# Kernel optimization log

Measured on AMD Instinct MI355X. Metric: run time of the kernel, lower is better.

The kernel has to match this reference:

```python
import jax, jax.numpy as jnp
import numpy as np
import math

B, S, HID, L, NH, V, M = 8, 512, 768, 12, 12, 30522, 512
FF = 4 * HID
D = HID // NH


def sinusoidal_pe(seq_len, dim):
    pos = np.arange(seq_len, dtype=np.float32)[:, None]
    i = np.arange(dim // 2, dtype=np.float32)[None, :]
    ang = pos / np.power(10000.0, 2.0 * i / dim)
    pe = np.zeros((seq_len, dim), np.float32)
    pe[:, 0::2] = np.sin(ang)
    pe[:, 1::2] = np.cos(ang)
    return jnp.asarray(pe)


def setup_inputs() -> dict:
    key = jax.random.key(0)
    ks = iter(jax.random.split(key, 32))
    g = lambda sh: jax.random.normal(next(ks), sh, jnp.float32) * 0.02
    return {
        "token_ids": jax.random.randint(next(ks), (B, S), 0, V),
        "segment_info": jax.random.randint(next(ks), (B, S), 0, 2),
        "tok_emb": g((V, HID)),
        "seg_emb": g((3, HID)),
        "Wq": g((L, HID, HID)), "bq": jnp.zeros((L, HID)),
        "Wk": g((L, HID, HID)), "bk": jnp.zeros((L, HID)),
        "Wv": g((L, HID, HID)), "bv": jnp.zeros((L, HID)),
        "Wo": g((L, HID, HID)), "bo": jnp.zeros((L, HID)),
        "Wpk": g((L, HID, HID)),
        "Wpq": g((L, HID, HID)),
        "rel_emb": g((L, 2 * M, HID)),
        "ln1_g": jnp.ones((L, HID)), "ln1_b": jnp.zeros((L, HID)),
        "ln2_g": jnp.ones((L, HID)), "ln2_b": jnp.zeros((L, HID)),
        "W1": g((L, HID, FF)), "b1": jnp.zeros((L, FF)),
        "W2": g((L, FF, HID)), "b2": jnp.zeros((L, HID)),
        "lnf_g": jnp.ones((HID,)), "lnf_b": jnp.zeros((HID,)),
    }


def _ln(x, g, b):
    mu = x.mean(-1, keepdims=True)
    var = ((x - mu) ** 2).mean(-1, keepdims=True)
    return (x - mu) * jax.lax.rsqrt(var + 1e-5) * g + b


def _forward(token_ids, segment_info, tok_emb, seg_emb, layer_params, lnf_g, lnf_b):
    mask = token_ids != 0  # [B,S] valid-key mask
    x = tok_emb[token_ids] + sinusoidal_pe(S, HID)[None] + seg_emb[segment_info]
    qidx = jnp.arange(S)[:, None]
    # relative position bucket: clamp(q-k, -M, M-1) + M  -> [0, 2M)
    rel = jnp.clip(qidx - jnp.arange(S)[None, :], -M, M - 1) + M  # [S,S]
    scale = 1.0 / math.sqrt(3.0 * D)  # DeBERTa scales by sqrt(3d) for 3 score terms

    def body(x, p):
        (Wq, bq, Wk, bk, Wv, bv, Wo, bo, Wpk, Wpq, rel_e,
         l1g, l1b, l2g, l2b, W1, b1, W2, b2) = p
        # pre-norm attention sublayer
        h = _ln(x, l1g, l1b)
        q = (h @ Wq + bq).reshape(B, S, NH, D)
        k = (h @ Wk + bk).reshape(B, S, NH, D)
        v = (h @ Wv + bv).reshape(B, S, NH, D)
        c2c = jnp.einsum('bqhd,bkhd->bhqk', q, k)
        pk = (rel_e @ Wpk).reshape(2 * M, NH, D)
        pq = (rel_e @ Wpq).reshape(2 * M, NH, D)
        # content-to-position: Q_q . posK[rel(q,k)]
        c2p = jnp.einsum('bqhd,rhd->bhqr', q, pk)[:, :, qidx, rel]  # [B,NH,S,S]
        # position-to-content: K_k . posQ[rel(k,q)] -> gather over k rows then transpose
        p2c = jnp.einsum('bkhd,rhd->bhkr', k, pq)[:, :, qidx, rel]  # [B,NH,k,q]
        scores = (c2c + c2p + jnp.swapaxes(p2c, -1, -2)) * scale
        scores = jnp.where(mask[:, None, None, :], scores, -1e9)
        attn = jax.nn.softmax(scores, axis=-1)
        ctx = jnp.einsum('bhqk,bkhd->bqhd', attn, v).reshape(B, S, HID)
        x = x + ctx @ Wo + bo
        # pre-norm feedforward sublayer
        h2 = _ln(x, l2g, l2b)
        x = x + jax.nn.gelu(h2 @ W1 + b1, approximate=False) @ W2 + b2
        return x, None

    x, _ = jax.lax.scan(body, x, layer_params)
    return _ln(x, lnf_g, lnf_b)


def reference(token_ids, segment_info, tok_emb, seg_emb, Wq, bq, Wk, bk, Wv, bv,
              Wo, bo, Wpk, Wpq, rel_emb, ln1_g, ln1_b, ln2_g, ln2_b,
              W1, b1, W2, b2, lnf_g, lnf_b):
    lp = (Wq, bq, Wk, bk, Wv, bv, Wo, bo, Wpk, Wpq, rel_emb,
          ln1_g, ln1_b, ln2_g, ln2_b, W1, b1, W2, b2)
    return _forward(token_ids, segment_info, tok_emb, seg_emb, lp, lnf_g, lnf_b)
```

## Files before the change

kernel.cpp:

```cpp
#include <hip/hip_runtime.h>
#include <hip/hip_bf16.h>
#include <cstddef>
#include <cstdint>


constexpr int B   = 8;
constexpr int S   = 512;
constexpr int HID = 768;
constexpr int L   = 12;
constexpr int NH  = 12;
constexpr int D   = 64;
constexpr int FF  = 3072;
constexpr int M2  = 1024;
constexpr int NTOK = B * S;

using f32x4 = __attribute__((ext_vector_type(4))) float;
using s16x8 = __attribute__((ext_vector_type(8))) short;
typedef unsigned short us;

__device__ inline float wave_sum(float v) {
#pragma unroll
  for (int o = 32; o > 0; o >>= 1) v += __shfl_xor(v, o, 64);
  return v;
}
__device__ inline us f2bf(float f) {
  __hip_bfloat16 h = __float2bfloat16(f);
  return *reinterpret_cast<us*>(&h);
}
__device__ inline float bf2f(us u) {
  union { unsigned int i; float f; } x;
  x.i = ((unsigned int)u) << 16;
  return x.f;
}
__device__ inline int swz8(int row, int g) {
  return row * 64 + ((g ^ (row & 7)) << 3);
}
#define GLOAD16(gp, lp)                                                  \
  __builtin_amdgcn_global_load_lds(                                     \
      (const __attribute__((address_space(1))) void*)(gp),              \
      (__attribute__((address_space(3))) void*)(lp), 16, 0, 0)

__global__ void embed_kernel(const int* __restrict__ tok,
                             const int* __restrict__ seg,
                             const float* __restrict__ tok_emb,
                             const float* __restrict__ seg_emb,
                             float* __restrict__ x) {
  int row = blockIdx.x;
  int s = row & (S - 1);
  int t = tok[row];
  int sg = seg[row];
  for (int c = threadIdx.x; c < HID; c += blockDim.x) {
    int i = c >> 1;
    float ang = (float)s * powf(10000.0f, -2.0f * (float)i / (float)HID);
    float pe = (c & 1) ? cosf(ang) : sinf(ang);
    x[(size_t)row * HID + c] = tok_emb[(size_t)t * HID + c] + pe
                             + seg_emb[(size_t)sg * HID + c];
  }
}

template <int BF16OUT>
__global__ __launch_bounds__(256)
void ln_kernel(const float* __restrict__ in, void* __restrict__ outp,
               const float* __restrict__ g, const float* __restrict__ b,
               int nrows) {
  int wave = threadIdx.x >> 6, lane = threadIdx.x & 63;
  int row = blockIdx.x * 4 + wave;
  if (row >= nrows) return;
  const float* xr = in + (size_t)row * HID;
  float v[12];
  float s = 0.f;
#pragma unroll
  for (int i = 0; i < 12; i++) { v[i] = xr[lane + i * 64]; s += v[i]; }
  s = wave_sum(s);
  float mu = s * (1.0f / HID);
  float ss = 0.f;
#pragma unroll
  for (int i = 0; i < 12; i++) { float d = v[i] - mu; ss += d * d; }
  ss = wave_sum(ss);
  float inv = rsqrtf(ss * (1.0f / HID) + 1e-5f);
#pragma unroll
  for (int i = 0; i < 12; i++) {
    int c = lane + i * 64;
    float o = (v[i] - mu) * inv * g[c] + b[c];
    if (BF16OUT)
      ((us*)outp)[(size_t)row * HID + c] = f2bf(o);
    else
      ((float*)outp)[(size_t)row * HID + c] = o;
  }
}

__global__ __launch_bounds__(256)
void weight_prep(const float* Wq, const float* Wk, const float* Wv,
                 const float* Wo, const float* Wpk, const float* Wpq,
                 const float* W1s, const float* W2s, const float* rel,
                 us* __restrict__ wt6, us* __restrict__ wt1,
                 us* __restrict__ wt2, us* __restrict__ rel16) {
  int bz = blockIdx.x;
  if (bz >= 8064) {
    int i = (bz - 8064) * 1024 + threadIdx.x * 4;
    f32x4 v = *(const f32x4*)&rel[i];
#pragma unroll
    for (int j = 0; j < 4; j++) rel16[i + j] = f2bf(v[j]);
    return;
  }
  __shared__ float tile[32][33];
  int tx = threadIdx.x & 31, ty = threadIdx.x >> 5;
  const float* src;
  us* dst;
  int N, K, nt, kt;
  if (bz < 3456) {
    int z = bz / 576, r = bz % 576;
    const float* srcs[6] = {Wq, Wk, Wv, Wo, Wpk, Wpq};
    src = srcs[z];
    dst = wt6 + (size_t)z * HID * HID;
    N = HID; K = HID;
    nt = (r % 24) * 32; kt = (r / 24) * 32;
  } else if (bz < 5760) {
    int r = bz - 3456;
    src = W1s; dst = wt1; N = FF; K = HID;
    nt = (r % 96) * 32; kt = (r / 96) * 32;
  } else {
    int r = bz - 5760;
    src = W2s; dst = wt2; N = HID; K = FF;
    nt = (r % 24) * 32; kt = (r / 24) * 32;
  }
#pragma unroll
  for (int i = 0; i < 4; i++)
    tile[ty + i * 8][tx] = src[(size_t)(kt + ty + i * 8) * N + nt + tx];
  __syncthreads();
#pragma unroll
  for (int i = 0; i < 4; i++)
    dst[(size_t)(nt + ty + i * 8) * K + kt + tx] = f2bf(tile[tx][ty + i * 8]);
}

__global__ void concat_bias(const float* __restrict__ bq,
                            const float* __restrict__ bk,
                            const float* __restrict__ bv,
                            float* __restrict__ bqkv) {
  int i = blockIdx.x * 256 + threadIdx.x;
  if (i >= L * 2304) return;
  int l = i / 2304, c = i % 2304;
  float v = (c < 768) ? bq[l * 768 + c]
          : (c < 1536) ? bk[l * 768 + c - 768] : bv[l * 768 + c - 1536];
  bqkv[i] = v;
}

template <int TN, int OUT_BF16, int GELU, int PARTIAL>
__global__ __launch_bounds__(256)
void mfma_gemm(const us* __restrict__ A, const us* __restrict__ Bt,
               const float* __restrict__ bias, const float* __restrict__ res,
               void* __restrict__ C, int Mr, int K, int N, int Kc) {
  constexpr int NW = TN / 32;
  __shared__ us As[128 * 32];
  __shared__ us Bs[TN * 32];
  int t = threadIdx.x, wave = t >> 6, lane = t & 63;
  int r0 = blockIdx.y * 128, n0 = blockIdx.x * TN;
  int kb = blockIdx.z * Kc;
  int wr = (wave >> 1) * 64;
  int wc = (wave & 1) * (TN / 2);

  f32x4 acc[4][NW] = {};
  int srow = lane >> 2, selem = (lane & 3) * 8;

  for (int k0 = kb; k0 < kb + Kc; k0 += 32) {
    __syncthreads();
    {
      const us* gA = A + (size_t)(r0 + wave * 32 + srow) * K + k0 + selem;
      us* lA = &As[(wave * 32) * 32];
      GLOAD16(gA, lA);
      GLOAD16(gA + (size_t)16 * K, lA + 16 * 32);
      if (TN == 128) {
        const us* gB = Bt + (size_t)(n0 + wave * 32 + srow) * K + k0 + selem;
        us* lB = &Bs[(wave * 32) * 32];
        GLOAD16(gB, lB);
        GLOAD16(gB + (size_t)16 * K, lB + 16 * 32);
      } else {
        const us* gB = Bt + (size_t)(n0 + wave * 16 + srow) * K + k0 + selem;
        GLOAD16(gB, &Bs[(wave * 16) * 32]);
      }
    }
    __syncthreads();

    s16x8 af[4], bf[NW];
#pragma unroll
    for (int m = 0; m < 4; m++)
      af[m] = *(const s16x8*)&As[(wr + m * 16 + (lane & 15)) * 32 + (lane >> 4) * 8];
#pragma unroll
    for (int n = 0; n < NW; n++)
      bf[n] = *(const s16x8*)&Bs[(wc + n * 16 + (lane & 15)) * 32 + (lane >> 4) * 8];
#pragma unroll
    for (int m = 0; m < 4; m++)
#pragma unroll
      for (int n = 0; n < NW; n++)
        acc[m][n] = __builtin_amdgcn_mfma_f32_16x16x32_bf16(af[m], bf[n],
                                                            acc[m][n], 0, 0, 0);
  }

  if (PARTIAL) {
    float* Cp = (float*)C + (size_t)blockIdx.z * Mr * N;
#pragma unroll
    for (int n = 0; n < NW; n++) {
      int c = n0 + wc + n * 16 + (lane & 15);
#pragma unroll
      for (int m = 0; m < 4; m++) {
        int rb = r0 + wr + m * 16 + ((lane >> 4) << 2);
#pragma unroll
        for (int j = 0; j < 4; j++)
          Cp[(size_t)(rb + j) * N + c] = acc[m][n][j];
      }
    }
    return;
  }
#pragma unroll
  for (int n = 0; n < NW; n++) {
    int c = n0 + wc + n * 16 + (lane & 15);
    float bv = bias ? bias[c] : 0.f;
#pragma unroll
    for (int m = 0; m < 4; m++) {
      int rb = r0 + wr + m * 16 + ((lane >> 4) << 2);
#pragma unroll
      for (int j = 0; j < 4; j++) {
        int r = rb + j;
        float val = acc[m][n][j] + bv;
        if (GELU) val = 0.5f * val * (1.0f + erff(val * 0.70710678118654752f));
        if (res)  val += res[(size_t)r * N + c];
        if (OUT_BF16)
          ((us*)C)[(size_t)r * N + c] = f2bf(val);
        else
          ((float*)C)[(size_t)r * N + c] = val;
      }
    }
  }
}

template <int LAST>
__global__ __launch_bounds__(256)
void combine_ln(const float* __restrict__ part,
                float* __restrict__ x, const float* __restrict__ bias,
                const float* __restrict__ g, const float* __restrict__ bb,
                void* __restrict__ outp) {
  int row = blockIdx.x, t = threadIdx.x;
  int wave = t >> 6, lane = t & 63;
  __shared__ float red[4];
  float v[3];
  float s = 0.f;
#pragma unroll
  for (int i = 0; i < 3; i++) {
    int c = t + i * 256;
    size_t idx = (size_t)row * HID + c;
    float val = x[idx] + part[idx] + part[(size_t)NTOK * HID + idx] + bias[c];
    if (!LAST) x[idx] = val;
    v[i] = val;
    s += val;
  }
  s = wave_sum(s);
  if (lane == 0) red[wave] = s;
  __syncthreads();
  float mu = (red[0] + red[1] + red[2] + red[3]) * (1.0f / HID);
  float ss = 0.f;
#pragma unroll
  for (int i = 0; i < 3; i++) { float d = v[i] - mu; ss += d * d; }
  ss = wave_sum(ss);
  __syncthreads();
  if (lane == 0) red[wave] = ss;
  __syncthreads();
  float inv = rsqrtf((red[0] + red[1] + red[2] + red[3]) * (1.0f / HID) + 1e-5f);
#pragma unroll
  for (int i = 0; i < 3; i++) {
    int c = t + i * 256;
    float o = (v[i] - mu) * inv * g[c] + bb[c];
    if (LAST)
      ((float*)outp)[(size_t)row * HID + c] = o;
    else
      ((us*)outp)[(size_t)row * HID + c] = f2bf(o);
  }
}

__global__ __launch_bounds__(256)
void transpose_v(const us* __restrict__ qkv, us* __restrict__ vt) {
  __shared__ us tile[32][34];
  int bh = blockIdx.z;
  int b = bh / NH, h = bh % NH;
  int s0 = blockIdx.x * 32, d0 = blockIdx.y * 32;
  int tx = threadIdx.x & 31, ty = threadIdx.x >> 5;
#pragma unroll
  for (int i = 0; i < 4; i++)
    tile[ty + i * 8][tx] =
        qkv[(size_t)(b * S + s0 + ty + i * 8) * 2304 + 1536 + h * 64 + d0 + tx];
  __syncthreads();
#pragma unroll
  for (int i = 0; i < 4; i++)
    vt[((size_t)bh * 64 + d0 + ty + i * 8) * S + s0 + tx] = tile[tx][ty + i * 8];
}

__global__ __launch_bounds__(256, 3)
void flash_attn(const us* __restrict__ qkv,
                const us* __restrict__ pkq,
                const us* __restrict__ vt,
                const int* __restrict__ tok,
                us* __restrict__ ctx) {
  constexpr int TS = 130;
  __shared__ us Ks[64 * 64];
  __shared__ us Vs[64 * 64];
  __shared__ us Band[16640];
  us* PKb = Band;
  us* PQb = Band + 8192;
  us* c2pL = Band;
  us* p2cL = Band + 8320;

  int t = threadIdx.x, wave = t >> 6, lane = t & 63;
  int bh = blockIdx.y;
  int b = bh / NH, h = bh % NH;
  int q0 = blockIdx.x * 64;
  int l15 = lane & 15, l4 = lane >> 4;
  const float scale = 0.07216878364870323f;

  s16x8 qf[2];
#pragma unroll
  for (int ks = 0; ks < 2; ks++)
    qf[ks] = *(const s16x8*)&qkv[(size_t)(b * S + q0 + wave * 16 + l15) * 2304
                                 + h * 64 + ks * 32 + l4 * 8];

  float m[4], l[4];
  f32x4 accO[4];
#pragma unroll
  for (int j = 0; j < 4; j++) { m[j] = -1e30f; l[j] = 0.f; }
#pragma unroll
  for (int n = 0; n < 4; n++) accO[n] = (f32x4){0.f, 0.f, 0.f, 0.f};

  for (int k0 = 0; k0 < S; k0 += 64) {
#pragma unroll
    for (int i = 0; i < 2; i++) {
      int c = t + i * 256;
      int r = c >> 3, g = c & 7;
      *(s16x8*)&Ks[swz8(r, g)] =
          *(const s16x8*)&qkv[(size_t)(b * S + k0 + r) * 2304 + 768 + h * 64 + g * 8];
      *(s16x8*)&Vs[swz8(r, g)] =
          *(const s16x8*)&vt[((size_t)bh * 64 + r) * S + k0 + g * 8];
    }
    int lo1 = q0 - k0 + 449;
    int lo2 = k0 - q0 + 449;
#pragma unroll
    for (int i = 0; i < 4; i++) {
      int c = t + i * 256;
      int r = c >> 3, g = c & 7;
      int r1 = lo1 + r; r1 = r1 < 0 ? 0 : (r1 > M2 - 1 ? M2 - 1 : r1);
      int r2 = lo2 + r; r2 = r2 < 0 ? 0 : (r2 > M2 - 1 ? M2 - 1 : r2);
      *(s16x8*)&PKb[swz8(r, g)] =
          *(const s16x8*)&pkq[(size_t)r1 * 1536 + h * 64 + g * 8];
      *(s16x8*)&PQb[swz8(r, g)] =
          *(const s16x8*)&pkq[(size_t)r2 * 1536 + 768 + h * 64 + g * 8];
    }
    __syncthreads();

    f32x4 c2c[4] = {};
    f32x4 cp[8] = {}, pc[8] = {};
#pragma unroll
    for (int ks = 0; ks < 2; ks++) {
      int g = ks * 4 + l4;
      int rA = wave * 16 + l15;
      s16x8 ak = *(const s16x8*)&Ks[swz8(rA, g)];
#pragma unroll
      for (int n = 0; n < 4; n++) {
        int rB = n * 16 + l15;
        s16x8 bk = *(const s16x8*)&Ks[swz8(rB, g)];
        c2c[n] = __builtin_amdgcn_mfma_f32_16x16x32_bf16(qf[ks], bk, c2c[n], 0, 0, 0);
      }
#pragma unroll
      for (int tt = 0; tt < 8; tt++) {
        int rr = tt * 16 + l15;
        s16x8 bpk = *(const s16x8*)&PKb[swz8(rr, g)];
        s16x8 bpq = *(const s16x8*)&PQb[swz8(rr, g)];
        cp[tt] = __builtin_amdgcn_mfma_f32_16x16x32_bf16(qf[ks], bpk, cp[tt], 0, 0, 0);
        pc[tt] = __builtin_amdgcn_mfma_f32_16x16x32_bf16(ak, bpq, pc[tt], 0, 0, 0);
      }
    }
    __syncthreads();

    {
      int rw = wave * 16 + (l4 << 2);
#pragma unroll
      for (int tt = 0; tt < 8; tt++)
#pragma unroll
        for (int j = 0; j < 4; j++) {
          c2pL[(rw + j) * TS + tt * 16 + l15] = f2bf(cp[tt][j]);
          p2cL[(rw + j) * TS + tt * 16 + l15] = f2bf(pc[tt][j]);
        }
    }
    __syncthreads();

    float p[4][4];
    float rmax[4];
#pragma unroll
    for (int j = 0; j < 4; j++) rmax[j] = -1e30f;
#pragma unroll
    for (int n = 0; n < 4; n++) {
      int ik = n * 16 + l15;
      bool msk = (tok[b * S + k0 + ik] == 0);
#pragma unroll
      for (int j = 0; j < 4; j++) {
        int iq = wave * 16 + (l4 << 2) + j;
        float sc = c2c[n][j]
                 + bf2f(c2pL[iq * TS + (iq - ik + 63)])
                 + bf2f(p2cL[ik * TS + (ik - iq + 63)]);
        sc *= scale;
        if (msk) sc = -1e9f;
        p[n][j] = sc;
        rmax[j] = fmaxf(rmax[j], sc);
      }
    }
#pragma unroll
    for (int o = 8; o > 0; o >>= 1)
#pragma unroll
      for (int j = 0; j < 4; j++)
        rmax[j] = fmaxf(rmax[j], __shfl_xor(rmax[j], o, 64));
    float al[4];
#pragma unroll
    for (int j = 0; j < 4; j++) {
      float mn = fmaxf(m[j], rmax[j]);
      al[j] = __expf(m[j] - mn);
      m[j] = mn;
    }
    float rs[4] = {0.f, 0.f, 0.f, 0.f};
#pragma unroll
    for (int n = 0; n < 4; n++)
#pragma unroll
      for (int j = 0; j < 4; j++) {
        p[n][j] = __expf(p[n][j] - m[j]);
        rs[j] += p[n][j];
      }
#pragma unroll
    for (int o = 8; o > 0; o >>= 1)
#pragma unroll
      for (int j = 0; j < 4; j++) rs[j] += __shfl_xor(rs[j], o, 64);
#pragma unroll
    for (int j = 0; j < 4; j++) l[j] = l[j] * al[j] + rs[j];
#pragma unroll
    for (int n = 0; n < 4; n++)
#pragma unroll
      for (int j = 0; j < 4; j++) accO[n][j] *= al[j];

    {
      int rw = wave * 16 + (l4 << 2);
#pragma unroll
      for (int n = 0; n < 4; n++)
#pragma unroll
        for (int j = 0; j < 4; j++) {
          int row = rw + j, col = n * 16 + l15;
          Ks[row * 64 + (((col >> 3) ^ (row & 7)) << 3) + (col & 7)] = f2bf(p[n][j]);
        }
    }
    __syncthreads();

#pragma unroll
    for (int ks = 0; ks < 2; ks++) {
      int g = ks * 4 + l4;
      int rA = wave * 16 + l15;
      s16x8 ap = *(const s16x8*)&Ks[swz8(rA, g)];
#pragma unroll
      for (int n = 0; n < 4; n++) {
        int rB = n * 16 + l15;
        s16x8 bv2 = *(const s16x8*)&Vs[swz8(rB, g)];
        accO[n] = __builtin_amdgcn_mfma_f32_16x16x32_bf16(ap, bv2, accO[n], 0, 0, 0);
      }
    }
    __syncthreads();
  }

#pragma unroll
  for (int n = 0; n < 4; n++) {
    int dd = h * 64 + n * 16 + l15;
#pragma unroll
    for (int j = 0; j < 4; j++) {
      int iq = q0 + wave * 16 + (l4 << 2) + j;
      ctx[(size_t)(b * S + iq) * HID + dd] = f2bf(accO[n][j] / l[j]);
    }
  }
}

extern "C" void kernel_launch(void* const* d_in, const int* in_sizes, int n_in,
                              void* d_out, int out_size, void* d_ws,
                              size_t ws_size, hipStream_t stream) {
  (void)in_sizes; (void)n_in; (void)out_size; (void)ws_size;
  const int*   tok     = (const int*)d_in[0];
  const int*   seg     = (const int*)d_in[1];
  const float* tok_emb = (const float*)d_in[2];
  const float* seg_emb = (const float*)d_in[3];
  const float* Wq  = (const float*)d_in[4];
  const float* bq  = (const float*)d_in[5];
  const float* Wk  = (const float*)d_in[6];
  const float* bk  = (const float*)d_in[7];
  const float* Wv  = (const float*)d_in[8];
  const float* bv  = (const float*)d_in[9];
  const float* Wo  = (const float*)d_in[10];
  const float* bo  = (const float*)d_in[11];
  const float* Wpk = (const float*)d_in[12];
  const float* Wpq = (const float*)d_in[13];
  const float* rel = (const float*)d_in[14];
  const float* ln1g = (const float*)d_in[15];
  const float* ln1b = (const float*)d_in[16];
  const float* ln2g = (const float*)d_in[17];
  const float* ln2b = (const float*)d_in[18];
  const float* W1  = (const float*)d_in[19];
  const float* b1  = (const float*)d_in[20];
  const float* W2  = (const float*)d_in[21];
  const float* b2  = (const float*)d_in[22];
  const float* lnfg = (const float*)d_in[23];
  const float* lnfb = (const float*)d_in[24];
  float* out = (float*)d_out;

  char* base = (char*)d_ws;
  size_t off = 0;
  auto alloc = [&](size_t bytes) -> void* {
    void* p = base + off;
    off += (bytes + 255) & ~(size_t)255;
    return p;
  };
  const size_t XSZ = (size_t)NTOK * HID;
  float* x = (float*)alloc(XSZ * 4);
  us* qkv16 = (us*)alloc((size_t)NTOK * 2304 * 2);
  us* pkq16 = (us*)alloc((size_t)M2 * 1536 * 2);
  us* vt16  = (us*)alloc(XSZ * 2);
  us* act16 = (us*)alloc(XSZ * 2);
  us* ff16  = (us*)alloc((size_t)NTOK * FF * 2);
  us* rel16 = (us*)alloc((size_t)M2 * HID * 2);
  us* wt6   = (us*)alloc((size_t)6 * HID * HID * 2);
  us* wt1   = (us*)alloc((size_t)HID * FF * 2);
  us* wt2   = (us*)alloc((size_t)HID * FF * 2);
  float* skbuf = (float*)alloc((size_t)2 * NTOK * HID * 4);
  float* bqkv  = (float*)alloc((size_t)L * 2304 * 4);

  const size_t WSQ = (size_t)HID * HID;

  embed_kernel<<<NTOK, 256, 0, stream>>>(tok, seg, tok_emb, seg_emb, x);
  concat_bias<<<(L * 2304 + 255) / 256, 256, 0, stream>>>(bq, bk, bv, bqkv);
  ln_kernel<1><<<NTOK / 4, 256, 0, stream>>>(x, act16, ln1g, ln1b, NTOK);

  for (int l = 0; l < L; l++) {
    weight_prep<<<8832, 256, 0, stream>>>(
        Wq + l * WSQ, Wk + l * WSQ, Wv + l * WSQ, Wo + l * WSQ,
        Wpk + l * WSQ, Wpq + l * WSQ, W1 + (size_t)l * HID * FF,
        W2 + (size_t)l * FF * HID, rel + (size_t)l * M2 * HID,
        wt6, wt1, wt2, rel16);

    mfma_gemm<128, 1, 0, 0><<<dim3(2304 / 128, NTOK / 128, 1), 256, 0, stream>>>(
        act16, wt6, bqkv + l * 2304, nullptr, qkv16, NTOK, HID, 2304, HID);
    mfma_gemm<64, 1, 0, 0><<<dim3(1536 / 64, M2 / 128, 1), 256, 0, stream>>>(
        rel16, wt6 + 4 * WSQ, nullptr, nullptr, pkq16, M2, HID, 1536, HID);
    transpose_v<<<dim3(S / 32, D / 32, B * NH), 256, 0, stream>>>(qkv16, vt16);
    flash_attn<<<dim3(S / 64, B * NH), 256, 0, stream>>>(
        qkv16, pkq16, vt16, tok, act16);
    mfma_gemm<64, 0, 0, 0><<<dim3(HID / 64, NTOK / 128, 1), 256, 0, stream>>>(
        act16, wt6 + 3 * WSQ, bo + l * HID, x, x, NTOK, HID, HID, HID);

    ln_kernel<1><<<NTOK / 4, 256, 0, stream>>>(x, act16, ln2g + l * HID,
                                               ln2b + l * HID, NTOK);
    mfma_gemm<128, 1, 1, 0><<<dim3(FF / 128, NTOK / 128, 1), 256, 0, stream>>>(
        act16, wt1, b1 + l * FF, nullptr, ff16, NTOK, HID, FF, HID);
    mfma_gemm<64, 0, 0, 1><<<dim3(HID / 64, NTOK / 128, 2), 256, 0, stream>>>(
        ff16, wt2, nullptr, nullptr, skbuf, NTOK, FF, HID, FF / 2);
    if (l < L - 1) {
      combine_ln<0><<<NTOK, 256, 0, stream>>>(
          skbuf, x, b2 + l * HID, ln1g + (l + 1) * HID, ln1b + (l + 1) * HID,
          act16);
    } else {
      combine_ln<1><<<NTOK, 256, 0, stream>>>(
          skbuf, x, b2 + l * HID, lnfg, lnfb, out);
    }
  }
}
```

Measured before the change: 4.069 ms.

## Precompute dense c2p/p2c position score matrices in separate kernel before attention

A new kernel computes the content-to-position and position-to-content products once per (query, relative offset) and writes them as dense [S,S] bf16 matrices into scratch buffers reused from the FFN intermediate and split-K buffers, four batches at a time. The attention kernel then loads 64x64 tiles of those matrices instead of recomputing 128-wide band MFMAs per key tile. This removes redundant band MFMA work and one LDS round-trip plus a barrier in the attention inner loop, and allows higher occupancy. The cost is extra global memory traffic for the precomputed matrices and extra kernel launches.

New measurement: 4.465 ms. 9.7% more time.

```diff
diff --git a/kernel.cpp b/kernel.cpp
--- a/kernel.cpp
+++ b/kernel.cpp
@@ -34,6 +34,9 @@
 }
 __device__ inline int swz8(int row, int g) {
   return row * 64 + ((g ^ (row & 7)) << 3);
+}
+__device__ inline int swze(int r, int c) {
+  return r * 64 + ((((c >> 3) ^ (r & 7)) << 3) | (c & 7));
 }
 #define GLOAD16(gp, lp)                                                  \
   __builtin_amdgcn_global_load_lds(                                     \
@@ -293,24 +296,85 @@
     vt[((size_t)bh * 64 + d0 + ty + i * 8) * S + s0 + tx] = tile[tx][ty + i * 8];
 }
 
-__global__ __launch_bounds__(256, 3)
+__global__ __launch_bounds__(256)
+void qpkp_kernel(const us* __restrict__ qkv, const us* __restrict__ pkq,
+                 us* __restrict__ QPh, us* __restrict__ KPh, int b0) {
+  __shared__ us As[64 * 64];
+  __shared__ us Bs[64 * 64];
+  int t = threadIdx.x, wave = t >> 6, lane = t & 63;
+  int l15 = lane & 15, l4 = lane >> 4;
+  int t0 = blockIdx.x * 64;
+  int bhl = blockIdx.y;
+  int b = b0 + bhl / NH, h = bhl % NH;
+  int z = blockIdx.z;
+  int zoff = z * 768;
+  us* outp = (z ? KPh : QPh) + ((size_t)bhl * 512 + t0) * 512;
+
+#pragma unroll
+  for (int i = 0; i < 2; i++) {
+    int c = t + i * 256;
+    int r = c >> 3, g = c & 7;
+    *(s16x8*)&As[swz8(r, g)] =
+        *(const s16x8*)&qkv[(size_t)(b * S + t0 + r) * 2304 + zoff + h * 64 + g * 8];
+  }
+
+  s16x8 af[2];
+  for (int c = 0; c < 9; c++) {
+#pragma unroll
+    for (int i = 0; i < 2; i++) {
+      int cc = t + i * 256;
+      int rr = cc >> 3, g = cc & 7;
+      int rb = t0 + 1 + c * 64 + rr;
+      rb = rb > M2 - 1 ? M2 - 1 : rb;
+      *(s16x8*)&Bs[swz8(rr, g)] =
+          *(const s16x8*)&pkq[(size_t)rb * 1536 + zoff + h * 64 + g * 8];
+    }
+    __syncthreads();
+    if (c == 0) {
+#pragma unroll
+      for (int ks = 0; ks < 2; ks++)
+        af[ks] = *(const s16x8*)&As[swz8(wave * 16 + l15, ks * 4 + l4)];
+    }
+    f32x4 acc[4] = {};
+#pragma unroll
+    for (int ks = 0; ks < 2; ks++)
+#pragma unroll
+      for (int n = 0; n < 4; n++) {
+        s16x8 bf = *(const s16x8*)&Bs[swz8(n * 16 + l15, ks * 4 + l4)];
+        acc[n] = __builtin_amdgcn_mfma_f32_16x16x32_bf16(af[ks], bf, acc[n], 0, 0, 0);
+      }
+#pragma unroll
+    for (int n = 0; n < 4; n++) {
+      int rcp = c * 64 + n * 16 + l15;
+#pragma unroll
+      for (int jj = 0; jj < 4; jj++) {
+        int iq = wave * 16 + (l4 << 2) + jj;
+        int j = rcp - iq;
+        if ((unsigned)j < 512u)
+          outp[(size_t)iq * 512 + j] = f2bf(acc[n][jj]);
+      }
+    }
+    __syncthreads();
+  }
+}
+
+__global__ __launch_bounds__(256, 4)
 void flash_attn(const us* __restrict__ qkv,
-                const us* __restrict__ pkq,
+                const us* __restrict__ QPh,
+                const us* __restrict__ KPh,
                 const us* __restrict__ vt,
                 const int* __restrict__ tok,
-                us* __restrict__ ctx) {
-  constexpr int TS = 130;
-  __shared__ us Ks[64 * 64];
-  __shared__ us Vs[64 * 64];
-  __shared__ us Band[16640];
-  us* PKb = Band;
-  us* PQb = Band + 8192;
-  us* c2pL = Band;
-  us* p2cL = Band + 8320;
+                us* __restrict__ ctx, int b0) {
+  __shared__ us Ks[4096];
+  __shared__ us Vs[4096];
+  __shared__ us QPs[4096];
+  __shared__ us KPs[4096];
+  __shared__ us Ps[4096];
 
   int t = threadIdx.x, wave = t >> 6, lane = t & 63;
-  int bh = blockIdx.y;
-  int b = bh / NH, h = bh % NH;
+  int bhl = blockIdx.y;
+  int b = b0 + bhl / NH, h = bhl % NH;
+  int bh = b * NH + h;
   int q0 = blockIdx.x * 64;
   int l15 = lane & 15, l4 = lane >> 4;
   const float scale = 0.07216878364870323f;
@@ -337,57 +401,23 @@
           *(const s16x8*)&qkv[(size_t)(b * S + k0 + r) * 2304 + 768 + h * 64 + g * 8];
       *(s16x8*)&Vs[swz8(r, g)] =
           *(const s16x8*)&vt[((size_t)bh * 64 + r) * S + k0 + g * 8];
-    }
-    int lo1 = q0 - k0 + 449;
-    int lo2 = k0 - q0 + 449;
-#pragma unroll
-    for (int i = 0; i < 4; i++) {
-      int c = t + i * 256;
-      int r = c >> 3, g = c & 7;
-      int r1 = lo1 + r; r1 = r1 < 0 ? 0 : (r1 > M2 - 1 ? M2 - 1 : r1);
-      int r2 = lo2 + r; r2 = r2 < 0 ? 0 : (r2 > M2 - 1 ? M2 - 1 : r2);
-      *(s16x8*)&PKb[swz8(r, g)] =
-          *(const s16x8*)&pkq[(size_t)r1 * 1536 + h * 64 + g * 8];
-      *(s16x8*)&PQb[swz8(r, g)] =
-          *(const s16x8*)&pkq[(size_t)r2 * 1536 + 768 + h * 64 + g * 8];
+      *(s16x8*)&QPs[swz8(r, g)] =
+          *(const s16x8*)&QPh[((size_t)bhl * 512 + q0 + r) * 512 + (448 - k0) + g * 8];
+      *(s16x8*)&KPs[swz8(r, g)] =
+          *(const s16x8*)&KPh[((size_t)bhl * 512 + k0 + r) * 512 + (448 - q0) + g * 8];
     }
     __syncthreads();
 
     f32x4 c2c[4] = {};
-    f32x4 cp[8] = {}, pc[8] = {};
 #pragma unroll
     for (int ks = 0; ks < 2; ks++) {
       int g = ks * 4 + l4;
-      int rA = wave * 16 + l15;
-      s16x8 ak = *(const s16x8*)&Ks[swz8(rA, g)];
 #pragma unroll
       for (int n = 0; n < 4; n++) {
-        int rB = n * 16 + l15;
-        s16x8 bk = *(const s16x8*)&Ks[swz8(rB, g)];
+        s16x8 bk = *(const s16x8*)&Ks[swz8(n * 16 + l15, g)];
         c2c[n] = __builtin_amdgcn_mfma_f32_16x16x32_bf16(qf[ks], bk, c2c[n], 0, 0, 0);
       }
-#pragma unroll
-      for (int tt = 0; tt < 8; tt++) {
-        int rr = tt * 16 + l15;
-        s16x8 bpk = *(const s16x8*)&PKb[swz8(rr, g)];
-        s16x8 bpq = *(const s16x8*)&PQb[swz8(rr, g)];
-        cp[tt] = __builtin_amdgcn_mfma_f32_16x16x32_bf16(qf[ks], bpk, cp[tt], 0, 0, 0);
-        pc[tt] = __builtin_amdgcn_mfma_f32_16x16x32_bf16(ak, bpq, pc[tt], 0, 0, 0);
-      }
-    }
-    __syncthreads();
-
-    {
-      int rw = wave * 16 + (l4 << 2);
-#pragma unroll
-      for (int tt = 0; tt < 8; tt++)
-#pragma unroll
-        for (int j = 0; j < 4; j++) {
-          c2pL[(rw + j) * TS + tt * 16 + l15] = f2bf(cp[tt][j]);
-          p2cL[(rw + j) * TS + tt * 16 + l15] = f2bf(pc[tt][j]);
-        }
-    }
-    __syncthreads();
+    }
 
     float p[4][4];
     float rmax[4];
@@ -397,12 +427,13 @@
     for (int n = 0; n < 4; n++) {
       int ik = n * 16 + l15;
       bool msk = (tok[b * S + k0 + ik] == 0);
+      int ccp = 63 - ik;
 #pragma unroll
       for (int j = 0; j < 4; j++) {
         int iq = wave * 16 + (l4 << 2) + j;
         float sc = c2c[n][j]
-                 + bf2f(c2pL[iq * TS + (iq - ik + 63)])
-                 + bf2f(p2cL[ik * TS + (ik - iq + 63)]);
+                 + bf2f(QPs[swze(iq, ccp)])
+                 + bf2f(KPs[swze(ik, 63 - iq)]);
         sc *= scale;
         if (msk) sc = -1e9f;
         p[n][j] = sc;
@@ -445,22 +476,18 @@
 #pragma unroll
       for (int n = 0; n < 4; n++)
 #pragma unroll
-        for (int j = 0; j < 4; j++) {
-          int row = rw + j, col = n * 16 + l15;
-          Ks[row * 64 + (((col >> 3) ^ (row & 7)) << 3) + (col & 7)] = f2bf(p[n][j]);
-        }
+        for (int j = 0; j < 4; j++)
+          Ps[swze(rw + j, n * 16 + l15)] = f2bf(p[n][j]);
     }
     __syncthreads();
 
 #pragma unroll
     for (int ks = 0; ks < 2; ks++) {
       int g = ks * 4 + l4;
-      int rA = wave * 16 + l15;
-      s16x8 ap = *(const s16x8*)&Ks[swz8(rA, g)];
+      s16x8 ap = *(const s16x8*)&Ps[swz8(wave * 16 + l15, g)];
 #pragma unroll
       for (int n = 0; n < 4; n++) {
-        int rB = n * 16 + l15;
-        s16x8 bv2 = *(const s16x8*)&Vs[swz8(rB, g)];
+        s16x8 bv2 = *(const s16x8*)&Vs[swz8(n * 16 + l15, g)];
         accO[n] = __builtin_amdgcn_mfma_f32_16x16x32_bf16(ap, bv2, accO[n], 0, 0, 0);
       }
     }
@@ -530,6 +557,9 @@
   float* skbuf = (float*)alloc((size_t)2 * NTOK * HID * 4);
   float* bqkv  = (float*)alloc((size_t)L * 2304 * 4);
 
+  us* QPh = ff16;
+  us* KPh = (us*)skbuf;
+
   const size_t WSQ = (size_t)HID * HID;
 
   embed_kernel<<<NTOK, 256, 0, stream>>>(tok, seg, tok_emb, seg_emb, x);
@@ -548,8 +578,12 @@
     mfma_gemm<64, 1, 0, 0><<<dim3(1536 / 64, M2 / 128, 1), 256, 0, stream>>>(
         rel16, wt6 + 4 * WSQ, nullptr, nullptr, pkq16, M2, HID, 1536, HID);
     transpose_v<<<dim3(S / 32, D / 32, B * NH), 256, 0, stream>>>(qkv16, vt16);
-    flash_attn<<<dim3(S / 64, B * NH), 256, 0, stream>>>(
-        qkv16, pkq16, vt16, tok, act16);
+    for (int b0 = 0; b0 < B; b0 += 4) {
+      qpkp_kernel<<<dim3(S / 64, 4 * NH, 2), 256, 0, stream>>>(
+          qkv16, pkq16, QPh, KPh, b0);
+      flash_attn<<<dim3(S / 64, 4 * NH), 256, 0, stream>>>(
+          qkv16, QPh, KPh, vt16, tok, act16, b0);
+    }
     mfma_gemm<64, 0, 0, 0><<<dim3(HID / 64, NTOK / 128, 1), 256, 0, stream>>>(
         act16, wt6 + 3 * WSQ, bo + l * HID, x, x, NTOK, HID, HID, HID);
 
```
